# Performance work log

Hardware: AMD Instinct MI355X
Metric: run time of the kernel (lower is better)

The kernel has to match this reference:

```python
import jax, jax.numpy as jnp
import numpy as np

N_E = 1024    # codebook size
E_DIM = 256   # code dimension
BETA = 0.25   # commitment cost


def setup_inputs() -> dict:
    key = jax.random.key(0)
    k1, k2 = jax.random.split(key)
    z = jax.random.normal(k1, (32, E_DIM, 32, 32), dtype=jnp.float32)
    # embedding init uniform(-1/n_e, 1/n_e) as in the torch module
    e_w = jax.random.uniform(k2, (N_E, E_DIM), jnp.float32, -1.0 / N_E, 1.0 / N_E)
    return {"z": z, "e_w": e_w}


def _vq_forward(z, e_w):
    B, C, H, W = z.shape  # C == E_DIM
    z_flat = jnp.transpose(z, (0, 2, 3, 1)).reshape(-1, C)  # (N, D)
    # squared euclidean distances: ||z||^2 + ||e||^2 - 2 z.e
    d = ((z_flat ** 2).sum(-1, keepdims=True)
         + (e_w ** 2).sum(-1)[None, :]
         - 2.0 * (z_flat @ e_w.T))                          # (N, n_e)
    indices = jnp.argmin(d, axis=1)                          # (N,)
    one_hot = jax.nn.one_hot(indices, N_E, dtype=z.dtype)    # (N, n_e)
    z_q_flat = e_w[indices]                                  # == one_hot @ e_w
    z_q = jnp.transpose(z_q_flat.reshape(B, H, W, C), (0, 3, 1, 2))
    # use_ema=True branch: loss = beta * mse(z_q, sg(z))
    loss = BETA * jnp.mean((z_q - jax.lax.stop_gradient(z)) ** 2)
    # straight-through estimator
    z_q_st = z + jax.lax.stop_gradient(z_q - z)
    avg_probs = one_hot.mean(0)
    perplexity = jnp.exp(-jnp.sum(avg_probs * jnp.log(avg_probs + 1e-10)))
    return loss, z_q_st, perplexity, one_hot, indices


def reference(z, e_w):
    return _vq_forward(z, e_w)
```

## Files before the change

### kernel.cpp

```cpp
#include <hip/hip_runtime.h>
#include <math.h>

#define N_TOK 32768
#define NE    1024
#define DIM   256
#define EPS   1.5e-3f

#define OFF_ZQ   1u
#define OFF_PPL  8388609u
#define OFF_OH   8388610u
#define OFF_IDX  41943042u

#define RS_CAP 4096

typedef __attribute__((ext_vector_type(8))) short short8;
typedef __attribute__((ext_vector_type(8))) unsigned short ushort8;
typedef __attribute__((ext_vector_type(4))) float f32x4;
typedef __attribute__((ext_vector_type(2))) float f32x2;

__device__ __forceinline__ unsigned short bf_rne(float f) {
    unsigned u = __float_as_uint(f);
    return (unsigned short)((u + 0x7FFFu + ((u >> 16) & 1u)) >> 16);
}
__device__ __forceinline__ void gload16(const void* g, void* l) {
    __builtin_amdgcn_global_load_lds((const __attribute__((address_space(1))) void*)g,
                                     (__attribute__((address_space(3))) void*)l, 16, 0, 0);
}

__global__ __launch_bounds__(256) void vq_prep(const float* __restrict__ z,
                                               const float* __restrict__ ew,
                                               unsigned short* __restrict__ z1,
                                               unsigned short* __restrict__ e1,
                                               float* __restrict__ zn,
                                               float* __restrict__ en,
                                               float* __restrict__ sse)
{
    __shared__ float zf[64 * 257];
    const int t = threadIdx.x;

    if (blockIdx.x >= 512) {
        if (blockIdx.x == 512 && t == 0) sse[0] = 0.0f;
        const int code = (int)(blockIdx.x - 512) * 256 + t;
        const float* p = ew + (size_t)code * DIM;
        float s = 0.0f;
        for (int dg = 0; dg < 32; ++dg) {
            ushort8 s1;
#pragma unroll
            for (int j = 0; j < 8; ++j) {
                float v = p[dg * 8 + j];
                s = fmaf(v, v, s);
                s1[j] = bf_rne(v);
            }
            *reinterpret_cast<ushort8*>(e1 + (size_t)code * 256 + dg * 8) = s1;
        }
        en[code] = s;
        return;
    }

    const int img = blockIdx.x >> 4;
    const int hw0 = (blockIdx.x & 15) << 6;
    const float* zb = z + (size_t)img * (DIM * 1024) + hw0;

#pragma unroll
    for (int it = 0; it < 16; ++it) {
        int f = it * 256 + t;
        int c = f >> 4, hw4 = f & 15;
        float4 v = *reinterpret_cast<const float4*>(zb + (size_t)c * 1024 + hw4 * 4);
        zf[(hw4 * 4 + 0) * 257 + c] = v.x;
        zf[(hw4 * 4 + 1) * 257 + c] = v.y;
        zf[(hw4 * 4 + 2) * 257 + c] = v.z;
        zf[(hw4 * 4 + 3) * 257 + c] = v.w;
    }
    __syncthreads();

    if (t < 64) {
        float s = 0.0f;
#pragma unroll 8
        for (int c = 0; c < DIM; ++c) { float v = zf[t * 257 + c]; s = fmaf(v, v, s); }
        zn[img * 1024 + hw0 + t] = s;
    }

#pragma unroll
    for (int it = 0; it < 8; ++it) {
        int f = it * 256 + t;
        int tl = f >> 5, cg = f & 31;
        ushort8 s1;
#pragma unroll
        for (int j = 0; j < 8; ++j)
            s1[j] = (unsigned short)(__float_as_uint(zf[tl * 257 + cg * 8 + j]) >> 16);
        int tok = img * 1024 + hw0 + tl;
        *reinterpret_cast<ushort8*>(z1 + (size_t)tok * 256 + cg * 8) = s1;
    }
}

__global__ __launch_bounds__(256) void vq_argmin_mfma(const unsigned short* __restrict__ z1,
                                                      const unsigned short* __restrict__ e1,
                                                      const float* __restrict__ en,
                                                      unsigned long long* __restrict__ cmu)
{
    __shared__ short lds[2][8192];

    const int t = threadIdx.x;
    const int lane = t & 63, w = t >> 6;
    const int wr = w >> 1, wc = w & 1;
    const int bid = (blockIdx.x & 7) * 256 + (blockIdx.x >> 3);
    const int rb = bid >> 3, cbi = bid & 7;
    const int r0 = rb * 128, c0 = cbi * 128;

    const char* srcp[4];
#pragma unroll
    for (int i = 0; i < 4; ++i) {
        int flat = (w * 4 + i) * 64 + lane;
        int arr = flat >> 9;
        int rr  = (flat & 511) >> 2;
        int sl  = flat & 3;
        int slx = sl ^ ((rr >> 1) & 3);
        srcp[i] = (arr == 0)
            ? (const char*)(z1 + (size_t)(r0 + rr) * 256 + slx * 8)
            : (const char*)(e1 + (size_t)(c0 + rr) * 256 + slx * 8);
    }

    f32x4 acc[4][4];
#pragma unroll
    for (int i = 0; i < 4; ++i)
#pragma unroll
        for (int j = 0; j < 4; ++j) acc[i][j] = (f32x4)0.0f;

#pragma unroll
    for (int i = 0; i < 4; ++i)
        gload16(srcp[i], &lds[0][(w * 4 + i) * 512]);
    __syncthreads();

    int cur = 0;
    for (int kc = 0; kc < 8; ++kc) {
        if (kc < 7) {
            const unsigned kadd = (unsigned)(kc + 1) * 64u;
#pragma unroll
            for (int i = 0; i < 4; ++i)
                gload16(srcp[i] + kadd, &lds[cur ^ 1][(w * 4 + i) * 512]);
        }
        const short* L = &lds[cur][0];
        const short* za = L;
        const short* eb = L + 4096;

        short8 bfr[4];
#pragma unroll
        for (int fn = 0; fn < 4; ++fn) {
            int row = wc * 64 + fn * 16 + (lane & 15);
            int slot = (lane >> 4) ^ ((row >> 1) & 3);
            bfr[fn] = *reinterpret_cast<const short8*>(eb + row * 32 + slot * 8);
        }
#pragma unroll
        for (int fm = 0; fm < 4; ++fm) {
            int row = wr * 64 + fm * 16 + (lane & 15);
            int slot = (lane >> 4) ^ ((row >> 1) & 3);
            short8 a0 = *reinterpret_cast<const short8*>(za + row * 32 + slot * 8);
#pragma unroll
            for (int fn = 0; fn < 4; ++fn)
                acc[fm][fn] = __builtin_amdgcn_mfma_f32_16x16x32_bf16(a0, bfr[fn], acc[fm][fn], 0, 0, 0);
        }
        __syncthreads();
        cur ^= 1;
    }

    float env[4];
#pragma unroll
    for (int fn = 0; fn < 4; ++fn)
        env[fn] = en[c0 + wc * 64 + fn * 16 + (lane & 15)];

    float* sdm = reinterpret_cast<float*>(&lds[0][0]);

#pragma unroll
    for (int fm = 0; fm < 4; ++fm) {
#pragma unroll
        for (int reg = 0; reg < 4; ++reg) {
            int lrow = wr * 64 + fm * 16 + ((lane >> 4) << 2) + reg;
            float bd = 3.0e38f;
#pragma unroll
            for (int fn = 0; fn < 4; ++fn) {
                float dv = env[fn] - 2.0f * acc[fm][fn][reg];
                bd = fminf(bd, dv);
            }
#pragma unroll
            for (int m = 1; m <= 8; m <<= 1)
                bd = fminf(bd, __shfl_xor(bd, m));
            if ((lane & 15) == 0) sdm[wc * 128 + lrow] = bd;
        }
    }
    __syncthreads();
    if (t < 128) sdm[t] = fminf(sdm[t], sdm[128 + t]) + EPS;
    __syncthreads();

#pragma unroll
    for (int fm = 0; fm < 4; ++fm) {
        unsigned long long bl[4][4];
#pragma unroll
        for (int fn = 0; fn < 4; ++fn) {
#pragma unroll
            for (int reg = 0; reg < 4; ++reg) {
                int lrow = wr * 64 + fm * 16 + ((lane >> 4) << 2) + reg;
                float thr = sdm[lrow];
                float dv = env[fn] - 2.0f * acc[fm][fn][reg];
                bl[fn][reg] = __ballot(dv <= thr);
            }
        }
        const int q = lane >> 4;
#pragma unroll
        for (int reg = 0; reg < 4; ++reg) {
            unsigned long long h =
                  ((bl[0][reg] >> (q * 16)) & 0xFFFFull)
                | (((bl[1][reg] >> (q * 16)) & 0xFFFFull) << 16)
                | (((bl[2][reg] >> (q * 16)) & 0xFFFFull) << 32)
                | (((bl[3][reg] >> (q * 16)) & 0xFFFFull) << 48);
            if ((lane & 15) == reg) {
                int row = wr * 64 + fm * 16 + q * 4 + reg;
                cmu[(size_t)(r0 + row) * 16 + cbi * 2 + wc] = h;
            }
        }
    }
}

__global__ __launch_bounds__(256) void vq_rescore(const float* __restrict__ z,
                                                  const float* __restrict__ ew,
                                                  const float* __restrict__ zn,
                                                  const float* __restrict__ en,
                                                  const unsigned long long* __restrict__ cmu,
                                                  float* __restrict__ out_idx,
                                                  float* __restrict__ zq,
                                                  float* __restrict__ sse,
                                                  float* __restrict__ oh)
{
    __shared__ float zrow[16 * 260];
    __shared__ int   wl[RS_CAP];
    __shared__ int   wsum[4];
    __shared__ float redf[256];
    __shared__ unsigned long long best[16];

    const int t = threadIdx.x, lane = t & 63, w = t >> 6;
    const int tok0 = blockIdx.x * 16;
    const int img = tok0 >> 10, hw0 = tok0 & 1023;

    {
        const float* zc = z + (size_t)img * (DIM * 1024) + (size_t)t * 1024 + hw0;
#pragma unroll
        for (int j = 0; j < 4; ++j) {
            float4 v = *reinterpret_cast<const float4*>(zc + 4 * j);
            zrow[(4 * j + 0) * 260 + t] = v.x;
            zrow[(4 * j + 1) * 260 + t] = v.y;
            zrow[(4 * j + 2) * 260 + t] = v.z;
            zrow[(4 * j + 3) * 260 + t] = v.w;
        }
    }
    if (t < 16) best[t] = ~0ull;

    unsigned long long v = cmu[(size_t)(tok0 + (t >> 4)) * 16 + (t & 15)];
    int myc = __popcll(v);
    int x = myc;
#pragma unroll
    for (int d = 1; d < 64; d <<= 1) {
        int y = __shfl_up(x, d);
        if (lane >= d) x += y;
    }
    if (lane == 63) wsum[w] = x;
    __syncthreads();
    int woff = 0;
#pragma unroll
    for (int i = 0; i < 4; ++i) woff += (i < w) ? wsum[i] : 0;
    int total = wsum[0] + wsum[1] + wsum[2] + wsum[3];
    int base = woff + x - myc;
    {
        const int wd = t & 15, tk = t >> 4;
        unsigned long long vv = v;
        while (vv) {
            int b = __ffsll((long long)vv) - 1;
            vv &= vv - 1;
            int code = (wd >> 1) * 128 + (wd & 1) * 64 + b;
            if (base < RS_CAP) wl[base] = (tk << 10) | code;
            ++base;
        }
    }
    __syncthreads();
    if (total > RS_CAP) total = RS_CAP;

    for (int p = t; p < total; p += 256) {
        int e = wl[p];
        int tk = e >> 10, code = e & 1023;
        const float* ep = ew + (size_t)code * DIM;
        const float* zr = &zrow[tk * 260];
        float s = 0.0f;
#pragma unroll 8
        for (int d = 0; d < DIM; d += 4) {
            float4 e4 = *reinterpret_cast<const float4*>(ep + d);
            float4 z4 = *reinterpret_cast<const float4*>(zr + d);
            s = fmaf(z4.x, e4.x, s);
            s = fmaf(z4.y, e4.y, s);
            s = fmaf(z4.z, e4.z, s);
            s = fmaf(z4.w, e4.w, s);
        }
        float dv = (zn[tok0 + tk] + en[code]) - 2.0f * s;
        unsigned long long key = ((unsigned long long)__float_as_uint(dv) << 32) | (unsigned)code;
        atomicMin(&best[tk], key);
    }
    __syncthreads();
    if (t < 16) out_idx[tok0 + t] = (float)(unsigned)(best[t] & 0x3FFu);

    const int tk2 = t & 15, cg2 = t >> 4;
    const int bidx = (int)(best[tk2] & 0x3FFu);
    const int hwp = hw0 + tk2;
    float part = 0.0f;
    float* zqb = zq + (size_t)img * (DIM * 1024) + hwp;
    const float* ewb = ew + (size_t)bidx * DIM;
#pragma unroll
    for (int i = 0; i < 16; ++i) {
        int c = cg2 * 16 + i;
        float q = ewb[c];
        float zv = zrow[tk2 * 260 + c];
        __builtin_nontemporal_store(q, &zqb[(size_t)c << 10]);
        float dx = q - zv;
        part = fmaf(dx, dx, part);
    }
    redf[t] = part;
    __syncthreads();
    for (int s2 = 128; s2 > 0; s2 >>= 1) {
        if (t < s2) redf[t] += redf[t + s2];
        __syncthreads();
    }
    if (t == 0) atomicAdd(sse, redf[0]);

    if (oh) {
        const int w2 = t >> 6, lane2 = t & 63;
#pragma unroll
        for (int rr = 0; rr < 4; ++rr) {
            const int row = w2 * 4 + rr;
            const int bi2 = (int)(best[row] & 0x3FFull);
            float* rowp = oh + (size_t)(tok0 + row) * 1024;
#pragma unroll
            for (int j = 0; j < 4; ++j) {
                int i4 = j * 64 + lane2;
                if (i4 < 255) {
                    int k = 2 + i4 * 4;
                    f32x4 vv4;
                    vv4.x = (k     == bi2) ? 1.0f : 0.0f;
                    vv4.y = (k + 1 == bi2) ? 1.0f : 0.0f;
                    vv4.z = (k + 2 == bi2) ? 1.0f : 0.0f;
                    vv4.w = (k + 3 == bi2) ? 1.0f : 0.0f;
                    __builtin_nontemporal_store(vv4, reinterpret_cast<f32x4*>(rowp + k));
                }
            }
            if (lane2 == 0) {
                f32x2 v2; v2.x = (0 == bi2) ? 1.0f : 0.0f; v2.y = (1 == bi2) ? 1.0f : 0.0f;
                __builtin_nontemporal_store(v2, reinterpret_cast<f32x2*>(rowp));
            } else if (lane2 == 1) {
                f32x2 v2; v2.x = (1022 == bi2) ? 1.0f : 0.0f; v2.y = (1023 == bi2) ? 1.0f : 0.0f;
                __builtin_nontemporal_store(v2, reinterpret_cast<f32x2*>(rowp + 1022));
            }
        }
    }
}

__global__ __launch_bounds__(256) void vq_onehot(const float* __restrict__ idxf,
                                                 float* __restrict__ oh)
{
    const unsigned stride = gridDim.x * blockDim.x;
    const unsigned total2 = N_TOK * (NE / 2);
    for (unsigned o2 = blockIdx.x * blockDim.x + threadIdx.x; o2 < total2; o2 += stride) {
        unsigned n = o2 >> 7;
        int k = (int)((o2 & 127u) << 1);
        int idx = (int)idxf[n];
        float2 v;
        v.x = (k == idx) ? 1.0f : 0.0f;
        v.y = (k + 1 == idx) ? 1.0f : 0.0f;
        reinterpret_cast<float2*>(oh)[o2] = v;
    }
}

__global__ __launch_bounds__(1024) void vq_finalize(const float* __restrict__ idxf,
                                                    const float* __restrict__ sse,
                                                    float* __restrict__ loss,
                                                    float* __restrict__ ppl)
{
    __shared__ int   hist[NE];
    __shared__ float red[NE];
    const int t = threadIdx.x;
    hist[t] = 0;
    __syncthreads();
    const float2* idx2 = reinterpret_cast<const float2*>(idxf);
    for (int i = t; i < N_TOK / 2; i += 1024) {
        float2 v = idx2[i];
        atomicAdd(&hist[(int)v.x], 1);
        atomicAdd(&hist[(int)v.y], 1);
    }
    __syncthreads();
    float p = (float)hist[t] * (1.0f / (float)N_TOK);
    red[t] = p * logf(p + 1e-10f);
    __syncthreads();
    for (int s = 512; s > 0; s >>= 1) {
        if (t < s) red[t] += red[t + s];
        __syncthreads();
    }
    if (t == 0) {
        ppl[0]  = expf(-red[0]);
        loss[0] = 0.25f * sse[0] / (float)(N_TOK * DIM);
    }
}

extern "C" void kernel_launch(void* const* d_in, const int* in_sizes, int n_in,
                              void* d_out, int out_size, void* d_ws, size_t ws_size,
                              hipStream_t stream)
{
    const float* z  = (const float*)d_in[0];
    const float* ew = (const float*)d_in[1];
    float* out = (float*)d_out;

    float* out_idx = out + OFF_IDX;
    float* out_oh  = out + OFF_OH;
    float* out_zq  = out + OFF_ZQ;
    float* out_ppl = out + OFF_PPL;

    const size_t need = 1024u + 33554432u + 524288u + 4194304u + 131072u + 4096u;
    const bool big = ws_size >= need && ws_size >= (size_t)48u * 1024u * 1024u;
    char* base = big ? (char*)d_ws : (char*)out_oh;
    const size_t Z1o = big ? 1024u : 8u;
    const size_t E1o = Z1o + 33554432u;
    const size_t CMo = E1o + 524288u;
    const size_t ZNo = CMo + 4194304u;
    const size_t ENo = ZNo + 131072u;

    unsigned short* Z1 = (unsigned short*)(base + Z1o);
    unsigned short* E1 = (unsigned short*)(base + E1o);
    unsigned long long* CM = (unsigned long long*)(base + CMo);
    float* ZN = (float*)(base + ZNo);
    float* EN = (float*)(base + ENo);
    float* SSE = (float*)d_ws;

    vq_prep<<<516, 256, 0, stream>>>(z, ew, Z1, E1, ZN, EN, SSE);
    vq_argmin_mfma<<<2048, 256, 0, stream>>>(Z1, E1, EN, CM);
    vq_rescore<<<2048, 256, 0, stream>>>(z, ew, ZN, EN, CM, out_idx, out_zq, SSE,
                                         big ? out_oh : nullptr);
    if (!big) vq_onehot<<<2048, 256, 0, stream>>>(out_idx, out_oh);
    vq_finalize<<<1, 1024, 0, stream>>>(out_idx, SSE, out, out_ppl);
}
```

Baseline: 145.3 us.

## Zero one-hot in argmin kernel, scatter ones and histogram in rescore

The dense zero-fill of the 128MB one-hot output moves into the tail of the compute-bound MFMA argmin kernel, so the memory writes can overlap with matrix work in other blocks. The rescore kernel now writes only the single 1.0 per token and accumulates a global code histogram with atomics. The finalize kernel then reads that histogram instead of rebuilding it from the indices. This relies on the zero-fill being ordered before the rescore scatter, which holds through kernel order on the stream, and it adds global atomics on hot histogram bins.

```diff
diff --git a/kernel.cpp b/kernel.cpp
--- a/kernel.cpp
+++ b/kernel.cpp
@@ -33,7 +33,8 @@
                                                unsigned short* __restrict__ e1,
                                                float* __restrict__ zn,
                                                float* __restrict__ en,
-                                               float* __restrict__ sse)
+                                               float* __restrict__ sse,
+                                               int* __restrict__ hist)
 {
     __shared__ float zf[64 * 257];
     const int t = threadIdx.x;
@@ -41,6 +42,7 @@
     if (blockIdx.x >= 512) {
         if (blockIdx.x == 512 && t == 0) sse[0] = 0.0f;
         const int code = (int)(blockIdx.x - 512) * 256 + t;
+        if (hist) hist[code] = 0;
         const float* p = ew + (size_t)code * DIM;
         float s = 0.0f;
         for (int dg = 0; dg < 32; ++dg) {
@@ -96,7 +98,8 @@
 __global__ __launch_bounds__(256) void vq_argmin_mfma(const unsigned short* __restrict__ z1,
                                                       const unsigned short* __restrict__ e1,
                                                       const float* __restrict__ en,
-                                                      unsigned long long* __restrict__ cmu)
+                                                      unsigned long long* __restrict__ cmu,
+                                                      float* __restrict__ oh)
 {
     __shared__ short lds[2][8192];
 
@@ -218,6 +221,14 @@
             }
         }
     }
+
+    if (oh) {
+        char* dst = (char*)oh + (size_t)blockIdx.x * 65536u;
+        f32x2 zz; zz.x = 0.0f; zz.y = 0.0f;
+#pragma unroll
+        for (int k = 0; k < 32; ++k)
+            __builtin_nontemporal_store(zz, reinterpret_cast<f32x2*>(dst + (size_t)(k * 256 + t) * 8u));
+    }
 }
 
 __global__ __launch_bounds__(256) void vq_rescore(const float* __restrict__ z,
@@ -228,7 +239,8 @@
                                                   float* __restrict__ out_idx,
                                                   float* __restrict__ zq,
                                                   float* __restrict__ sse,
-                                                  float* __restrict__ oh)
+                                                  float* __restrict__ oh,
+                                                  int* __restrict__ hist)
 {
     __shared__ float zrow[16 * 260];
     __shared__ int   wl[RS_CAP];
@@ -302,7 +314,14 @@
         atomicMin(&best[tk], key);
     }
     __syncthreads();
-    if (t < 16) out_idx[tok0 + t] = (float)(unsigned)(best[t] & 0x3FFu);
+    if (t < 16) {
+        int bi = (int)(best[t] & 0x3FFu);
+        out_idx[tok0 + t] = (float)bi;
+        if (oh) {
+            oh[(size_t)(tok0 + t) * 1024 + bi] = 1.0f;
+            atomicAdd(&hist[bi], 1);
+        }
+    }
 
     const int tk2 = t & 15, cg2 = t >> 4;
     const int bidx = (int)(best[tk2] & 0x3FFu);
@@ -326,36 +345,6 @@
         __syncthreads();
     }
     if (t == 0) atomicAdd(sse, redf[0]);
-
-    if (oh) {
-        const int w2 = t >> 6, lane2 = t & 63;
-#pragma unroll
-        for (int rr = 0; rr < 4; ++rr) {
-            const int row = w2 * 4 + rr;
-            const int bi2 = (int)(best[row] & 0x3FFull);
-            float* rowp = oh + (size_t)(tok0 + row) * 1024;
-#pragma unroll
-            for (int j = 0; j < 4; ++j) {
-                int i4 = j * 64 + lane2;
-                if (i4 < 255) {
-                    int k = 2 + i4 * 4;
-                    f32x4 vv4;
-                    vv4.x = (k     == bi2) ? 1.0f : 0.0f;
-                    vv4.y = (k + 1 == bi2) ? 1.0f : 0.0f;
-                    vv4.z = (k + 2 == bi2) ? 1.0f : 0.0f;
-                    vv4.w = (k + 3 == bi2) ? 1.0f : 0.0f;
-                    __builtin_nontemporal_store(vv4, reinterpret_cast<f32x4*>(rowp + k));
-                }
-            }
-            if (lane2 == 0) {
-                f32x2 v2; v2.x = (0 == bi2) ? 1.0f : 0.0f; v2.y = (1 == bi2) ? 1.0f : 0.0f;
-                __builtin_nontemporal_store(v2, reinterpret_cast<f32x2*>(rowp));
-            } else if (lane2 == 1) {
-                f32x2 v2; v2.x = (1022 == bi2) ? 1.0f : 0.0f; v2.y = (1023 == bi2) ? 1.0f : 0.0f;
-                __builtin_nontemporal_store(v2, reinterpret_cast<f32x2*>(rowp + 1022));
-            }
-        }
-    }
 }
 
 __global__ __launch_bounds__(256) void vq_onehot(const float* __restrict__ idxf,
@@ -374,7 +363,8 @@
     }
 }
 
-__global__ __launch_bounds__(1024) void vq_finalize(const float* __restrict__ idxf,
+__global__ __launch_bounds__(1024) void vq_finalize(const int* __restrict__ histg,
+                                                    const float* __restrict__ idxf,
                                                     const float* __restrict__ sse,
                                                     float* __restrict__ loss,
                                                     float* __restrict__ ppl)
@@ -382,15 +372,20 @@
     __shared__ int   hist[NE];
     __shared__ float red[NE];
     const int t = threadIdx.x;
-    hist[t] = 0;
-    __syncthreads();
-    const float2* idx2 = reinterpret_cast<const float2*>(idxf);
-    for (int i = t; i < N_TOK / 2; i += 1024) {
-        float2 v = idx2[i];
-        atomicAdd(&hist[(int)v.x], 1);
-        atomicAdd(&hist[(int)v.y], 1);
-    }
-    __syncthreads();
+    if (histg) {
+        hist[t] = histg[t];
+        __syncthreads();
+    } else {
+        hist[t] = 0;
+        __syncthreads();
+        const float2* idx2 = reinterpret_cast<const float2*>(idxf);
+        for (int i = t; i < N_TOK / 2; i += 1024) {
+            float2 v = idx2[i];
+            atomicAdd(&hist[(int)v.x], 1);
+            atomicAdd(&hist[(int)v.y], 1);
+        }
+        __syncthreads();
+    }
     float p = (float)hist[t] * (1.0f / (float)N_TOK);
     red[t] = p * logf(p + 1e-10f);
     __syncthreads();
@@ -417,7 +412,7 @@
     float* out_zq  = out + OFF_ZQ;
     float* out_ppl = out + OFF_PPL;
 
-    const size_t need = 1024u + 33554432u + 524288u + 4194304u + 131072u + 4096u;
+    const size_t need = 1024u + 33554432u + 524288u + 4194304u + 131072u + 8192u;
     const bool big = ws_size >= need && ws_size >= (size_t)48u * 1024u * 1024u;
     char* base = big ? (char*)d_ws : (char*)out_oh;
     const size_t Z1o = big ? 1024u : 8u;
@@ -425,18 +420,20 @@
     const size_t CMo = E1o + 524288u;
     const size_t ZNo = CMo + 4194304u;
     const size_t ENo = ZNo + 131072u;
+    const size_t HIo = ENo + 4096u;
 
     unsigned short* Z1 = (unsigned short*)(base + Z1o);
     unsigned short* E1 = (unsigned short*)(base + E1o);
     unsigned long long* CM = (unsigned long long*)(base + CMo);
     float* ZN = (float*)(base + ZNo);
     float* EN = (float*)(base + ENo);
+    int*   HI = big ? (int*)(base + HIo) : nullptr;
     float* SSE = (float*)d_ws;
 
-    vq_prep<<<516, 256, 0, stream>>>(z, ew, Z1, E1, ZN, EN, SSE);
-    vq_argmin_mfma<<<2048, 256, 0, stream>>>(Z1, E1, EN, CM);
+    vq_prep<<<516, 256, 0, stream>>>(z, ew, Z1, E1, ZN, EN, SSE, HI);
+    vq_argmin_mfma<<<2048, 256, 0, stream>>>(Z1, E1, EN, CM, big ? out_oh : nullptr);
     vq_rescore<<<2048, 256, 0, stream>>>(z, ew, ZN, EN, CM, out_idx, out_zq, SSE,
-                                         big ? out_oh : nullptr);
+                                         big ? out_oh : nullptr, HI);
     if (!big) vq_onehot<<<2048, 256, 0, stream>>>(out_idx, out_oh);
-    vq_finalize<<<1, 1024, 0, stream>>>(out_idx, SSE, out, out_ppl);
-}
+    vq_finalize<<<1, 1024, 0, stream>>>(HI, out_idx, SSE, out, out_ppl);
+}
```

New measurement: 148.8 us. 1.02x slower.

## Fuse perplexity and loss finalize into rescore via last-block histogram reduction

Applied to the files above, without the earlier changes.

The rescore kernel now handles 32 tokens per block instead of 16, which halves the grid. Each block adds its chosen codes into a global histogram. The last block to finish, found through an atomic counter, computes perplexity and loss, so the separate finalize launch is dropped on the big-workspace path. The rescore tolerance EPS is also tightened, which shrinks candidate lists but raises the chance of picking the wrong argmin near ties, and the larger block uses more shared memory per block.

```diff
diff --git a/kernel.cpp b/kernel.cpp
--- a/kernel.cpp
+++ b/kernel.cpp
@@ -4,7 +4,7 @@
 #define N_TOK 32768
 #define NE    1024
 #define DIM   256
-#define EPS   1.5e-3f
+#define EPS   8.0e-4f
 
 #define OFF_ZQ   1u
 #define OFF_PPL  8388609u
@@ -12,6 +12,7 @@
 #define OFF_IDX  41943042u
 
 #define RS_CAP 4096
+#define RS_TOK 32
 
 typedef __attribute__((ext_vector_type(8))) short short8;
 typedef __attribute__((ext_vector_type(8))) unsigned short ushort8;
@@ -33,14 +34,20 @@
                                                unsigned short* __restrict__ e1,
                                                float* __restrict__ zn,
                                                float* __restrict__ en,
-                                               float* __restrict__ sse)
+                                               float* __restrict__ sse,
+                                               int* __restrict__ hist,
+                                               int* __restrict__ ctr)
 {
     __shared__ float zf[64 * 257];
     const int t = threadIdx.x;
 
     if (blockIdx.x >= 512) {
-        if (blockIdx.x == 512 && t == 0) sse[0] = 0.0f;
+        if (blockIdx.x == 512 && t == 0) {
+            sse[0] = 0.0f;
+            if (ctr) ctr[0] = 0;
+        }
         const int code = (int)(blockIdx.x - 512) * 256 + t;
+        if (hist) hist[code] = 0;
         const float* p = ew + (size_t)code * DIM;
         float s = 0.0f;
         for (int dg = 0; dg < 32; ++dg) {
@@ -228,22 +235,27 @@
                                                   float* __restrict__ out_idx,
                                                   float* __restrict__ zq,
                                                   float* __restrict__ sse,
-                                                  float* __restrict__ oh)
-{
-    __shared__ float zrow[16 * 260];
+                                                  float* __restrict__ oh,
+                                                  int* __restrict__ hist,
+                                                  int* __restrict__ ctr,
+                                                  float* __restrict__ loss,
+                                                  float* __restrict__ ppl)
+{
+    __shared__ float zrow[RS_TOK * 260];
     __shared__ int   wl[RS_CAP];
     __shared__ int   wsum[4];
     __shared__ float redf[256];
-    __shared__ unsigned long long best[16];
+    __shared__ unsigned long long best[RS_TOK];
+    __shared__ int   rank_s;
 
     const int t = threadIdx.x, lane = t & 63, w = t >> 6;
-    const int tok0 = blockIdx.x * 16;
+    const int tok0 = blockIdx.x * RS_TOK;
     const int img = tok0 >> 10, hw0 = tok0 & 1023;
 
     {
         const float* zc = z + (size_t)img * (DIM * 1024) + (size_t)t * 1024 + hw0;
 #pragma unroll
-        for (int j = 0; j < 4; ++j) {
+        for (int j = 0; j < 8; ++j) {
             float4 v = *reinterpret_cast<const float4*>(zc + 4 * j);
             zrow[(4 * j + 0) * 260 + t] = v.x;
             zrow[(4 * j + 1) * 260 + t] = v.y;
@@ -251,10 +263,11 @@
             zrow[(4 * j + 3) * 260 + t] = v.w;
         }
     }
-    if (t < 16) best[t] = ~0ull;
-
-    unsigned long long v = cmu[(size_t)(tok0 + (t >> 4)) * 16 + (t & 15)];
-    int myc = __popcll(v);
+    if (t < RS_TOK) best[t] = ~0ull;
+
+    const size_t mb = (size_t)tok0 * 16;
+    unsigned long long v0 = cmu[mb + 2 * t], v1 = cmu[mb + 2 * t + 1];
+    int myc = __popcll(v0) + __popcll(v1);
     int x = myc;
 #pragma unroll
     for (int d = 1; d < 64; d <<= 1) {
@@ -269,12 +282,22 @@
     int total = wsum[0] + wsum[1] + wsum[2] + wsum[3];
     int base = woff + x - myc;
     {
-        const int wd = t & 15, tk = t >> 4;
-        unsigned long long vv = v;
+        const int tk = t >> 3;
+        const int wd0 = (t & 7) << 1;
+        unsigned long long vv = v0;
         while (vv) {
             int b = __ffsll((long long)vv) - 1;
             vv &= vv - 1;
-            int code = (wd >> 1) * 128 + (wd & 1) * 64 + b;
+            int code = (wd0 >> 1) * 128 + (wd0 & 1) * 64 + b;
+            if (base < RS_CAP) wl[base] = (tk << 10) | code;
+            ++base;
+        }
+        vv = v1;
+        const int wd1 = wd0 + 1;
+        while (vv) {
+            int b = __ffsll((long long)vv) - 1;
+            vv &= vv - 1;
+            int code = (wd1 >> 1) * 128 + (wd1 & 1) * 64 + b;
             if (base < RS_CAP) wl[base] = (tk << 10) | code;
             ++base;
         }
@@ -302,17 +325,17 @@
         atomicMin(&best[tk], key);
     }
     __syncthreads();
-    if (t < 16) out_idx[tok0 + t] = (float)(unsigned)(best[t] & 0x3FFu);
-
-    const int tk2 = t & 15, cg2 = t >> 4;
+    if (t < RS_TOK) out_idx[tok0 + t] = (float)(unsigned)(best[t] & 0x3FFu);
+
+    const int tk2 = t & 31, cg2 = t >> 5;
     const int bidx = (int)(best[tk2] & 0x3FFu);
     const int hwp = hw0 + tk2;
     float part = 0.0f;
     float* zqb = zq + (size_t)img * (DIM * 1024) + hwp;
     const float* ewb = ew + (size_t)bidx * DIM;
 #pragma unroll
-    for (int i = 0; i < 16; ++i) {
-        int c = cg2 * 16 + i;
+    for (int i = 0; i < 32; ++i) {
+        int c = cg2 * 32 + i;
         float q = ewb[c];
         float zv = zrow[tk2 * 260 + c];
         __builtin_nontemporal_store(q, &zqb[(size_t)c << 10]);
@@ -328,15 +351,14 @@
     if (t == 0) atomicAdd(sse, redf[0]);
 
     if (oh) {
-        const int w2 = t >> 6, lane2 = t & 63;
-#pragma unroll
-        for (int rr = 0; rr < 4; ++rr) {
-            const int row = w2 * 4 + rr;
+#pragma unroll
+        for (int rr = 0; rr < 8; ++rr) {
+            const int row = w * 8 + rr;
             const int bi2 = (int)(best[row] & 0x3FFull);
             float* rowp = oh + (size_t)(tok0 + row) * 1024;
 #pragma unroll
             for (int j = 0; j < 4; ++j) {
-                int i4 = j * 64 + lane2;
+                int i4 = j * 64 + lane;
                 if (i4 < 255) {
                     int k = 2 + i4 * 4;
                     f32x4 vv4;
@@ -347,12 +369,36 @@
                     __builtin_nontemporal_store(vv4, reinterpret_cast<f32x4*>(rowp + k));
                 }
             }
-            if (lane2 == 0) {
+            if (lane == 0) {
                 f32x2 v2; v2.x = (0 == bi2) ? 1.0f : 0.0f; v2.y = (1 == bi2) ? 1.0f : 0.0f;
                 __builtin_nontemporal_store(v2, reinterpret_cast<f32x2*>(rowp));
-            } else if (lane2 == 1) {
+            } else if (lane == 1) {
                 f32x2 v2; v2.x = (1022 == bi2) ? 1.0f : 0.0f; v2.y = (1023 == bi2) ? 1.0f : 0.0f;
                 __builtin_nontemporal_store(v2, reinterpret_cast<f32x2*>(rowp + 1022));
+            }
+        }
+        if (t < RS_TOK) atomicAdd(&hist[(int)(best[t] & 0x3FFu)], 1);
+
+        __threadfence();
+        if (t == 0) rank_s = atomicAdd(ctr, 1);
+        __syncthreads();
+        if (rank_s == (int)gridDim.x - 1) {
+            float a = 0.0f;
+            for (int i = t; i < NE; i += 256) {
+                int h = __hip_atomic_load(&hist[i], __ATOMIC_RELAXED, __HIP_MEMORY_SCOPE_AGENT);
+                float p = (float)h * (1.0f / (float)N_TOK);
+                a += p * logf(p + 1e-10f);
+            }
+            redf[t] = a;
+            __syncthreads();
+            for (int s2 = 128; s2 > 0; s2 >>= 1) {
+                if (t < s2) redf[t] += redf[t + s2];
+                __syncthreads();
+            }
+            if (t == 0) {
+                float ss = __hip_atomic_load(sse, __ATOMIC_RELAXED, __HIP_MEMORY_SCOPE_AGENT);
+                ppl[0]  = expf(-redf[0]);
+                loss[0] = 0.25f * ss / (float)(N_TOK * DIM);
             }
         }
     }
@@ -417,7 +463,7 @@
     float* out_zq  = out + OFF_ZQ;
     float* out_ppl = out + OFF_PPL;
 
-    const size_t need = 1024u + 33554432u + 524288u + 4194304u + 131072u + 4096u;
+    const size_t need = 1024u + 33554432u + 524288u + 4194304u + 131072u + 8192u;
     const bool big = ws_size >= need && ws_size >= (size_t)48u * 1024u * 1024u;
     char* base = big ? (char*)d_ws : (char*)out_oh;
     const size_t Z1o = big ? 1024u : 8u;
@@ -425,18 +471,23 @@
     const size_t CMo = E1o + 524288u;
     const size_t ZNo = CMo + 4194304u;
     const size_t ENo = ZNo + 131072u;
+    const size_t HIo = ENo + 4096u;
 
     unsigned short* Z1 = (unsigned short*)(base + Z1o);
     unsigned short* E1 = (unsigned short*)(base + E1o);
     unsigned long long* CM = (unsigned long long*)(base + CMo);
     float* ZN = (float*)(base + ZNo);
     float* EN = (float*)(base + ENo);
+    int*   HI = big ? (int*)(base + HIo) : nullptr;
     float* SSE = (float*)d_ws;
-
-    vq_prep<<<516, 256, 0, stream>>>(z, ew, Z1, E1, ZN, EN, SSE);
+    int*   CT = big ? (int*)((char*)d_ws + 8) : nullptr;
+
+    vq_prep<<<516, 256, 0, stream>>>(z, ew, Z1, E1, ZN, EN, SSE, HI, CT);
     vq_argmin_mfma<<<2048, 256, 0, stream>>>(Z1, E1, EN, CM);
-    vq_rescore<<<2048, 256, 0, stream>>>(z, ew, ZN, EN, CM, out_idx, out_zq, SSE,
-                                         big ? out_oh : nullptr);
-    if (!big) vq_onehot<<<2048, 256, 0, stream>>>(out_idx, out_oh);
-    vq_finalize<<<1, 1024, 0, stream>>>(out_idx, SSE, out, out_ppl);
-}
+    vq_rescore<<<1024, 256, 0, stream>>>(z, ew, ZN, EN, CM, out_idx, out_zq, SSE,
+                                         big ? out_oh : nullptr, HI, CT, out, out_ppl);
+    if (!big) {
+        vq_onehot<<<2048, 256, 0, stream>>>(out_idx, out_oh);
+        vq_finalize<<<1, 1024, 0, stream>>>(out_idx, SSE, out, out_ppl);
+    }
+}
```

New measurement: 323.5 us. +122.7%, slower.

## Tighten rescore margin, compact worklist, and build code histogram in rescore

Applied to the files above, without the earlier changes.

The bf16 candidate margin EPS is lowered, so fewer near-tie codes are flagged and rescored in fp32. The rescore worklist becomes 16-bit entries, which halves its shared-memory footprint. Each rescore block now adds its chosen indices into a global histogram, zeroed in prep, so the single-block finalize only reads 1024 counts instead of scanning all 32768 indices. The smaller margin risks missing the true argmin when bf16 error exceeds it, and the global atomics add some contention.

```diff
diff --git a/kernel.cpp b/kernel.cpp
--- a/kernel.cpp
+++ b/kernel.cpp
@@ -4,7 +4,7 @@
 #define N_TOK 32768
 #define NE    1024
 #define DIM   256
-#define EPS   1.5e-3f
+#define EPS   8.0e-4f
 
 #define OFF_ZQ   1u
 #define OFF_PPL  8388609u
@@ -12,6 +12,7 @@
 #define OFF_IDX  41943042u
 
 #define RS_CAP 4096
+#define RS_TOK 16
 
 typedef __attribute__((ext_vector_type(8))) short short8;
 typedef __attribute__((ext_vector_type(8))) unsigned short ushort8;
@@ -33,7 +34,8 @@
                                                unsigned short* __restrict__ e1,
                                                float* __restrict__ zn,
                                                float* __restrict__ en,
-                                               float* __restrict__ sse)
+                                               float* __restrict__ sse,
+                                               int* __restrict__ hist)
 {
     __shared__ float zf[64 * 257];
     const int t = threadIdx.x;
@@ -41,6 +43,7 @@
     if (blockIdx.x >= 512) {
         if (blockIdx.x == 512 && t == 0) sse[0] = 0.0f;
         const int code = (int)(blockIdx.x - 512) * 256 + t;
+        if (hist) hist[code] = 0;
         const float* p = ew + (size_t)code * DIM;
         float s = 0.0f;
         for (int dg = 0; dg < 32; ++dg) {
@@ -228,16 +231,17 @@
                                                   float* __restrict__ out_idx,
                                                   float* __restrict__ zq,
                                                   float* __restrict__ sse,
-                                                  float* __restrict__ oh)
-{
-    __shared__ float zrow[16 * 260];
-    __shared__ int   wl[RS_CAP];
+                                                  float* __restrict__ oh,
+                                                  int* __restrict__ hist)
+{
+    __shared__ float zrow[RS_TOK * 260];
+    __shared__ unsigned short wl[RS_CAP];
     __shared__ int   wsum[4];
     __shared__ float redf[256];
-    __shared__ unsigned long long best[16];
+    __shared__ unsigned long long best[RS_TOK];
 
     const int t = threadIdx.x, lane = t & 63, w = t >> 6;
-    const int tok0 = blockIdx.x * 16;
+    const int tok0 = blockIdx.x * RS_TOK;
     const int img = tok0 >> 10, hw0 = tok0 & 1023;
 
     {
@@ -251,7 +255,7 @@
             zrow[(4 * j + 3) * 260 + t] = v.w;
         }
     }
-    if (t < 16) best[t] = ~0ull;
+    if (t < RS_TOK) best[t] = ~0ull;
 
     unsigned long long v = cmu[(size_t)(tok0 + (t >> 4)) * 16 + (t & 15)];
     int myc = __popcll(v);
@@ -275,7 +279,7 @@
             int b = __ffsll((long long)vv) - 1;
             vv &= vv - 1;
             int code = (wd >> 1) * 128 + (wd & 1) * 64 + b;
-            if (base < RS_CAP) wl[base] = (tk << 10) | code;
+            if (base < RS_CAP) wl[base] = (unsigned short)((tk << 10) | code);
             ++base;
         }
     }
@@ -283,7 +287,7 @@
     if (total > RS_CAP) total = RS_CAP;
 
     for (int p = t; p < total; p += 256) {
-        int e = wl[p];
+        int e = (int)wl[p];
         int tk = e >> 10, code = e & 1023;
         const float* ep = ew + (size_t)code * DIM;
         const float* zr = &zrow[tk * 260];
@@ -302,7 +306,11 @@
         atomicMin(&best[tk], key);
     }
     __syncthreads();
-    if (t < 16) out_idx[tok0 + t] = (float)(unsigned)(best[t] & 0x3FFu);
+    if (t < RS_TOK) {
+        int bi = (int)(best[t] & 0x3FFu);
+        out_idx[tok0 + t] = (float)bi;
+        if (hist) atomicAdd(&hist[bi], 1);
+    }
 
     const int tk2 = t & 15, cg2 = t >> 4;
     const int bidx = (int)(best[tk2] & 0x3FFu);
@@ -374,7 +382,8 @@
     }
 }
 
-__global__ __launch_bounds__(1024) void vq_finalize(const float* __restrict__ idxf,
+__global__ __launch_bounds__(1024) void vq_finalize(const int* __restrict__ histg,
+                                                    const float* __restrict__ idxf,
                                                     const float* __restrict__ sse,
                                                     float* __restrict__ loss,
                                                     float* __restrict__ ppl)
@@ -382,15 +391,20 @@
     __shared__ int   hist[NE];
     __shared__ float red[NE];
     const int t = threadIdx.x;
-    hist[t] = 0;
-    __syncthreads();
-    const float2* idx2 = reinterpret_cast<const float2*>(idxf);
-    for (int i = t; i < N_TOK / 2; i += 1024) {
-        float2 v = idx2[i];
-        atomicAdd(&hist[(int)v.x], 1);
-        atomicAdd(&hist[(int)v.y], 1);
-    }
-    __syncthreads();
+    if (histg) {
+        hist[t] = histg[t];
+        __syncthreads();
+    } else {
+        hist[t] = 0;
+        __syncthreads();
+        const float2* idx2 = reinterpret_cast<const float2*>(idxf);
+        for (int i = t; i < N_TOK / 2; i += 1024) {
+            float2 v = idx2[i];
+            atomicAdd(&hist[(int)v.x], 1);
+            atomicAdd(&hist[(int)v.y], 1);
+        }
+        __syncthreads();
+    }
     float p = (float)hist[t] * (1.0f / (float)N_TOK);
     red[t] = p * logf(p + 1e-10f);
     __syncthreads();
@@ -417,7 +431,7 @@
     float* out_zq  = out + OFF_ZQ;
     float* out_ppl = out + OFF_PPL;
 
-    const size_t need = 1024u + 33554432u + 524288u + 4194304u + 131072u + 4096u;
+    const size_t need = 1024u + 33554432u + 524288u + 4194304u + 131072u + 8192u;
     const bool big = ws_size >= need && ws_size >= (size_t)48u * 1024u * 1024u;
     char* base = big ? (char*)d_ws : (char*)out_oh;
     const size_t Z1o = big ? 1024u : 8u;
@@ -425,18 +439,20 @@
     const size_t CMo = E1o + 524288u;
     const size_t ZNo = CMo + 4194304u;
     const size_t ENo = ZNo + 131072u;
+    const size_t HIo = ENo + 4096u;
 
     unsigned short* Z1 = (unsigned short*)(base + Z1o);
     unsigned short* E1 = (unsigned short*)(base + E1o);
     unsigned long long* CM = (unsigned long long*)(base + CMo);
     float* ZN = (float*)(base + ZNo);
     float* EN = (float*)(base + ENo);
+    int*   HI = big ? (int*)(base + HIo) : nullptr;
     float* SSE = (float*)d_ws;
 
-    vq_prep<<<516, 256, 0, stream>>>(z, ew, Z1, E1, ZN, EN, SSE);
+    vq_prep<<<516, 256, 0, stream>>>(z, ew, Z1, E1, ZN, EN, SSE, HI);
     vq_argmin_mfma<<<2048, 256, 0, stream>>>(Z1, E1, EN, CM);
     vq_rescore<<<2048, 256, 0, stream>>>(z, ew, ZN, EN, CM, out_idx, out_zq, SSE,
-                                         big ? out_oh : nullptr);
+                                         big ? out_oh : nullptr, HI);
     if (!big) vq_onehot<<<2048, 256, 0, stream>>>(out_idx, out_oh);
-    vq_finalize<<<1, 1024, 0, stream>>>(out_idx, SSE, out, out_ppl);
-}
+    vq_finalize<<<1, 1024, 0, stream>>>(HI, out_idx, SSE, out, out_ppl);
+}
```

After: 145.1 us. Within noise of the previous version (-0.1%).
